# Kernel tuning notes

Hardware: AMD Instinct MI355X
Metric: run time of the kernel (lower is better)

Reference implementation:

```python
import jax, jax.numpy as jnp
import numpy as np

TOPK = 60            # candidates kept by top-k
THRESHOLD = 0.15     # score threshold (post-sigmoid)
NMS_THRESHOLD = 0.05 # IoU overlap for suppression/matching
NMS_TOPK = 20        # max kept detections per image
CROP_SIZE = (96, 96, 96)
AVG_TOPN = 7         # max matched boxes averaged per kept box


def setup_inputs() -> dict:
    key = jax.random.key(0)
    k1, k2, k3 = jax.random.split(key, 3)
    B, D, H, W = 256, 24, 24, 24
    Cls = jax.random.normal(k1, (B, 1, D, H, W), dtype=jnp.float32)
    # sizes in [1,7) voxels so 3D boxes at stride-4 anchor spacing overlap
    Shape = jax.random.uniform(k2, (B, 3, D, H, W), dtype=jnp.float32) * 6.0 + 1.0
    Offset = jax.random.normal(k3, (B, 3, D, H, W), dtype=jnp.float32)
    return {"Cls": Cls, "Shape": Shape, "Offset": Offset}


def _decode(Cls, Shape, Offset):
    # make_anchors + bbox_decode: centers = (anchor + offset) * stride, sizes = Shape
    B, _, D, H, W = Cls.shape
    stride = jnp.float32(CROP_SIZE[0] / D)  # 96/24 = 4
    gz, gy, gx = jnp.meshgrid(jnp.arange(D, dtype=jnp.float32),
                              jnp.arange(H, dtype=jnp.float32),
                              jnp.arange(W, dtype=jnp.float32), indexing="ij")
    anchors = jnp.stack([gz, gy, gx], -1).reshape(-1, 3)            # [N,3]
    scores = jax.nn.sigmoid(Cls.reshape(B, -1))                     # [B,N] (is_logits=True)
    shapes = Shape.reshape(B, 3, -1).transpose(0, 2, 1)             # [B,N,3]
    offsets = Offset.reshape(B, 3, -1).transpose(0, 2, 1)           # [B,N,3]
    centers = (anchors[None] + offsets) * stride
    bboxes = jnp.concatenate([centers, shapes], -1)                 # [B,N,6] = (z,y,x,d,h,w)
    return scores, bboxes


def _iou_matrix(det):
    # axis-aligned 3D IoU between all pairs of the TOPK candidate boxes
    c, s = det[:, 2:5], det[:, 5:8]
    lo, hi = c - 0.5 * s, c + 0.5 * s
    inter = jnp.prod(jnp.maximum(jnp.minimum(hi[:, None], hi[None]) -
                                 jnp.maximum(lo[:, None], lo[None]), 0.0), -1)
    vol = jnp.prod(s, -1)
    return inter / (vol[:, None] + vol[None] - inter)


def _nms_image(scores, bboxes):
    # top-k (sorted descending, as torch.topk) then masked iterative NMS with
    # IoU-matched top-7 box averaging, emitting a fixed [NMS_TOPK, 8] table.
    topk_s, topk_i = jax.lax.top_k(scores, TOPK)
    valid = topk_s > THRESHOLD
    det = jnp.concatenate([jnp.ones((TOPK, 1), jnp.float32),
                           topk_s[:, None], bboxes[topk_i]], -1)    # [TOPK,8]
    iou = _iou_matrix(det)
    ar = jnp.arange(TOPK)

    def step(suppressed, _):
        avail = valid & ~suppressed
        any_avail = jnp.any(avail)
        idx = jnp.argmax(avail)  # first available = highest remaining score
        matched = avail & ((iou[idx] > NMS_THRESHOLD) | (ar == idx))
        rank = jnp.cumsum(matched) - 1            # matched are already score-sorted
        sel = matched & (rank < AVG_TOPN)
        top_n = jnp.minimum(jnp.sum(matched), AVG_TOPN)
        avg = jnp.sum(det * sel[:, None].astype(det.dtype), 0) / jnp.maximum(top_n, 1).astype(det.dtype)
        avg = avg.at[0].set(1.0).at[1].set(det[idx, 1])  # flag=1, prob = best score
        row = jnp.where(top_n > 1, avg, det[idx])
        row = jnp.where(any_avail, row, -jnp.ones(8, det.dtype))
        suppressed = jnp.where(any_avail, suppressed | matched, suppressed)
        return suppressed, row

    _, rows = jax.lax.scan(step, jnp.zeros(TOPK, dtype=bool), None, length=NMS_TOPK)
    return rows  # [NMS_TOPK, 8]


def reference(Cls, Shape, Offset):
    scores, bboxes = _decode(Cls, Shape, Offset)
    return jax.vmap(_nms_image)(scores, bboxes)  # [B, NMS_TOPK, 8]
```

## Files before the change

### kernel.cpp

```cpp
#include <hip/hip_runtime.h>
#include <math.h>

#define N_ANCH 13824
#define TPB 256
#define K_TOP 60
#define K_NMS 20
#define AVG_TOPN 7
#define SLOTS 12
#define PIVOT_KEY 0xC0100000u

__device__ __forceinline__ unsigned mono_key(float x) {
  unsigned m = __float_as_uint(x);
  return (m & 0x80000000u) ? ~m : (m | 0x80000000u);
}

__global__ __launch_bounds__(TPB)
void detpp_kernel(const float* __restrict__ Cls,
                  const float* __restrict__ Shp,
                  const float* __restrict__ Off,
                  float* __restrict__ Out) {
  __shared__ unsigned long long cand2[TPB * SLOTS];
  __shared__ float det[K_TOP][9];
  __shared__ unsigned long long Mrow[K_TOP];
  __shared__ unsigned int hist[4][256];
  __shared__ unsigned long long cand[64];
  __shared__ unsigned long long selk[64];
  __shared__ unsigned int ccnt, totcnt, oflow;
  __shared__ unsigned int g_prefix, g_r;

  const int b = blockIdx.x;
  const int t = threadIdx.x;
  const int lane = t & 63;
  const size_t cbase = (size_t)b * N_ANCH;

  if (t == 0) { ccnt = 0; totcnt = 0; oflow = 0; g_prefix = 0u; g_r = K_TOP; }
  if (t < K_TOP) Mrow[t] = 1ull << t;
  hist[0][t] = 0; hist[1][t] = 0; hist[2][t] = 0; hist[3][t] = 0;

  const float4* C4 = (const float4*)(Cls + cbase);
  float4 v[14];
  #pragma unroll
  for (int j = 0; j < 13; ++j) v[j] = C4[(j << 8) + t];
  if (t < 128) v[13] = C4[3328 + t];

  int cnt = 0;
  const int base = t * SLOTS;
  auto process = [&](float4 val, int i0) {
    float a[4] = {val.x, val.y, val.z, val.w};
    #pragma unroll
    for (int q = 0; q < 4; ++q) {
      unsigned k = mono_key(a[q]);
      if (k > PIVOT_KEY) {
        if (cnt < SLOTS)
          cand2[base + cnt] = ((unsigned long long)k << 32) | (unsigned)(~(i0 + q));
        cnt++;
      }
    }
  };
  #pragma unroll
  for (int j = 0; j < 13; ++j) process(v[j], ((j << 8) + t) << 2);
  if (t < 128) process(v[13], (3328 + t) << 2);

  int wsum = cnt;
  #pragma unroll
  for (int d = 1; d < 64; d <<= 1) wsum += __shfl_xor(wsum, d, 64);
  unsigned long long ofm = __ballot(cnt > SLOTS);
  if (lane == 0) {
    atomicAdd(&totcnt, (unsigned)wsum);
    if (ofm) atomicOr(&oflow, 1u);
  }
  __syncthreads();
  const unsigned total = totcnt;
  const bool fast = (total >= (unsigned)K_TOP) && (oflow == 0u);
  const int myn = cnt < SLOTS ? cnt : SLOTS;

  #pragma unroll
  for (int pass = 0; pass < 4; ++pass) {
    const int shift = 24 - 8 * pass;
    const unsigned pref = g_prefix;
    const unsigned rr = g_r;
    if (fast) {
      for (int kk = 0; kk < myn; ++kk) {
        unsigned k = (unsigned)(cand2[base + kk] >> 32);
        bool match;
        if (pass == 0) match = true;
        else match = (((k ^ pref) >> (shift + 8)) == 0u);
        if (match) atomicAdd(&hist[pass][(k >> shift) & 0xffu], 1u);
      }
    } else {
      for (int j = 0; j < 54; ++j) {
        int i = (j << 8) | t;
        unsigned k = mono_key(Cls[cbase + i]);
        bool match;
        if (pass == 0) match = true;
        else match = (((k ^ pref) >> (shift + 8)) == 0u);
        if (match) atomicAdd(&hist[pass][(k >> shift) & 0xffu], 1u);
      }
    }
    __syncthreads();
    if (t < 64) {
      unsigned c0 = hist[pass][4 * lane + 0], c1 = hist[pass][4 * lane + 1];
      unsigned c2 = hist[pass][4 * lane + 2], c3 = hist[pass][4 * lane + 3];
      unsigned pre1 = c0, pre2 = c0 + c1, pre3 = pre2 + c2, pre4 = pre3 + c3;
      unsigned S = pre4;
      #pragma unroll
      for (int d = 1; d < 64; d <<= 1) {
        unsigned o = __shfl_down(S, d, 64);
        if (lane + d < 64) S += o;
      }
      unsigned pre[5] = {0u, pre1, pre2, pre3, pre4};
      int mybin = -1;
      #pragma unroll
      for (int kk = 3; kk >= 0; --kk) {
        if (mybin < 0 && S - pre[kk] >= rr) mybin = kk;
      }
      unsigned long long m = __ballot(mybin >= 0);
      int hl = 63 - __builtin_clzll(m);
      if (lane == hl) {
        g_prefix = pref | ((unsigned)(4 * lane + mybin) << shift);
        g_r = rr - (S - pre[mybin + 1]);
      }
    }
    __syncthreads();
  }

  const unsigned K60 = g_prefix;
  if (fast) {
    for (int kk = 0; kk < myn; ++kk) {
      unsigned long long e = cand2[base + kk];
      if ((unsigned)(e >> 32) >= K60) {
        unsigned pos = atomicAdd(&ccnt, 1u);
        if (pos < 64) cand[pos] = e;
      }
    }
  } else {
    for (int j = 0; j < 54; ++j) {
      int i = (j << 8) | t;
      unsigned k = mono_key(Cls[cbase + i]);
      if (k >= K60) {
        unsigned pos = atomicAdd(&ccnt, 1u);
        if (pos < 64) cand[pos] = ((unsigned long long)k << 32) | (unsigned)(~i);
      }
    }
  }
  __syncthreads();

  if (t < 64) {
    unsigned cc = ccnt; if (cc > 64u) cc = 64u;
    unsigned long long klong = (lane < (int)cc) ? cand[lane] : 0ull;
    unsigned long long vv = ~klong;
    #pragma unroll
    for (int k = 2; k <= 64; k <<= 1) {
      #pragma unroll
      for (int j = k >> 1; j > 0; j >>= 1) {
        unsigned long long o = __shfl_xor(vv, j, 64);
        bool i_lower = ((lane & j) == 0);
        bool asc = ((lane & k) == 0);
        bool keep_min = (asc == i_lower);
        bool take = keep_min ? (o < vv) : (o > vv);
        if (take) vv = o;
      }
    }
    selk[lane] = ~vv;
  }
  __syncthreads();

  if (t < 180) {
    int e = t / 3;
    int f = t - 3 * e;
    unsigned long long kl = selk[e];
    int i = (int)(~(unsigned)(kl & 0xffffffffull));
    int iz = i / 576;
    int r2 = i - iz * 576;
    int iy = r2 / 24;
    int ix = r2 - iy * 24;
    int a = (f == 0) ? iz : ((f == 1) ? iy : ix);
    size_t bb = (size_t)b * 3 * N_ANCH + (size_t)f * N_ANCH + (size_t)i;
    float o = Off[bb];
    float s = Shp[bb];
    det[e][2 + f] = ((float)a + o) * 4.0f;
    det[e][5 + f] = s;
  } else if (t < 240) {
    int e = t - 180;
    unsigned long long kl = selk[e];
    unsigned m = (unsigned)(kl >> 32);
    unsigned bits = (m & 0x80000000u) ? (m & 0x7fffffffu) : ~m;
    float lg = __uint_as_float(bits);
    det[e][0] = 1.0f;
    det[e][1] = 1.0f / (1.0f + expf(-lg));
  }
  __syncthreads();

  for (int p = t; p < 1800; p += TPB) {
    int ii = p / 30;
    int k  = p - ii * 30;
    int jj = ii + 1 + k; if (jj >= 60) jj -= 60;
    float cz1 = det[ii][2], cy1 = det[ii][3], cx1 = det[ii][4];
    float sz1 = det[ii][5], sy1 = det[ii][6], sx1 = det[ii][7];
    float cz2 = det[jj][2], cy2 = det[jj][3], cx2 = det[jj][4];
    float sz2 = det[jj][5], sy2 = det[jj][6], sx2 = det[jj][7];
    float lz1 = cz1 - 0.5f * sz1, hz1 = cz1 + 0.5f * sz1;
    float ly1 = cy1 - 0.5f * sy1, hy1 = cy1 + 0.5f * sy1;
    float lx1 = cx1 - 0.5f * sx1, hx1 = cx1 + 0.5f * sx1;
    float lz2 = cz2 - 0.5f * sz2, hz2 = cz2 + 0.5f * sz2;
    float ly2 = cy2 - 0.5f * sy2, hy2 = cy2 + 0.5f * sy2;
    float lx2 = cx2 - 0.5f * sx2, hx2 = cx2 + 0.5f * sx2;
    float dz = fmaxf(fminf(hz1, hz2) - fmaxf(lz1, lz2), 0.0f);
    float dy = fmaxf(fminf(hy1, hy2) - fmaxf(ly1, ly2), 0.0f);
    float dx = fmaxf(fminf(hx1, hx2) - fmaxf(lx1, lx2), 0.0f);
    float inter = (dz * dy) * dx;
    float v1 = (sz1 * sy1) * sx1;
    float v2 = (sz2 * sy2) * sx2;
    float iouv = inter / (v1 + v2 - inter);
    if (iouv > 0.05f) {
      atomicOr(&Mrow[ii], 1ull << jj);
      atomicOr(&Mrow[jj], 1ull << ii);
    }
  }
  __syncthreads();

  if (t < 64) {
    const bool in = (lane < K_TOP);
    float myscore = in ? det[lane][1] : 0.0f;
    unsigned long long M = in ? Mrow[lane] : 0ull;
    unsigned long long validm = __ballot(in && (myscore > 0.15f));
    unsigned long long suppressed = 0ull;
    float* outb = Out + (size_t)b * K_NMS * 8;
    const int q = lane >> 3, c = lane & 7;

    #pragma unroll
    for (int step = 0; step < K_NMS; ++step) {
      unsigned long long avail = validm & ~suppressed;
      const bool any = (avail != 0ull);
      int idx = any ? (int)__builtin_ctzll(avail) : 0;
      unsigned mlo = (unsigned)__builtin_amdgcn_readlane((int)(unsigned)(M & 0xffffffffull), idx);
      unsigned mhi = (unsigned)__builtin_amdgcn_readlane((int)(unsigned)(M >> 32), idx);
      unsigned long long matched = any ? (avail & (((unsigned long long)mhi << 32) | mlo)) : 0ull;
      int cm = __popcll(matched);
      int top_n = cm < AVG_TOPN ? cm : AVG_TOPN;
      int myb = 0;
      { unsigned long long m2 = matched;
        #pragma unroll
        for (int z = 0; z < 8; ++z) {
          int bz = m2 ? (int)__builtin_ctzll(m2) : 0;
          if (z == q) myb = bz;
          m2 &= m2 - 1ull;
        } }
      float vv = (q < top_n) ? det[myb][c] : 0.0f;
      vv += __shfl_xor(vv, 8, 64);
      vv += __shfl_xor(vv, 16, 64);
      vv += __shfl_xor(vv, 32, 64);
      float sidx = __uint_as_float((unsigned)__builtin_amdgcn_readlane((int)__float_as_uint(myscore), idx));
      float r = vv / (float)(top_n > 0 ? top_n : 1);
      if (lane < 8) {
        float o = r;
        if (lane == 0) o = 1.0f;
        if (lane == 1) o = sidx;
        if (!any) o = -1.0f;
        outb[step * 8 + lane] = o;
      }
      suppressed |= matched;
    }
  }
}

extern "C" void kernel_launch(void* const* d_in, const int* in_sizes, int n_in,
                              void* d_out, int out_size, void* d_ws, size_t ws_size,
                              hipStream_t stream) {
  const float* Cls = (const float*)d_in[0];
  const float* Shp = (const float*)d_in[1];
  const float* Off = (const float*)d_in[2];
  float* Out = (float*)d_out;
  int B = in_sizes[0] / N_ANCH;
  detpp_kernel<<<B, TPB, 0, stream>>>(Cls, Shp, Off, Out);
}
```

Baseline: 123.2 us.

## Replace radix-select top-k with compacted candidate list and rank-by-count selection

Raises the block to 1024 threads and compacts every above-pivot logit into one shared list using a wave prefix scan, with a single atomic per wave. The four-pass histogram radix select and bitonic sort are replaced by rank counting: each candidate counts how many list entries beat it and writes its decoded box straight to that rank if it ranks below 60. This removes several barrier-separated passes and shared-memory histogram atomics. In exchange the counting is quadratic in the list size, and the fallback path is an O(N²) global-memory scan that would be very slow if ever taken.

```diff
diff --git a/kernel.cpp b/kernel.cpp
--- a/kernel.cpp
+++ b/kernel.cpp
@@ -2,11 +2,11 @@
 #include <math.h>
 
 #define N_ANCH 13824
-#define TPB 256
+#define TPB 1024
 #define K_TOP 60
 #define K_NMS 20
 #define AVG_TOPN 7
-#define SLOTS 12
+#define CAP 2048
 #define PIVOT_KEY 0xC0100000u
 
 __device__ __forceinline__ unsigned mono_key(float x) {
@@ -19,182 +19,129 @@
                   const float* __restrict__ Shp,
                   const float* __restrict__ Off,
                   float* __restrict__ Out) {
-  __shared__ unsigned long long cand2[TPB * SLOTS];
+  __shared__ unsigned long long list[CAP];
   __shared__ float det[K_TOP][9];
   __shared__ unsigned long long Mrow[K_TOP];
-  __shared__ unsigned int hist[4][256];
-  __shared__ unsigned long long cand[64];
-  __shared__ unsigned long long selk[64];
-  __shared__ unsigned int ccnt, totcnt, oflow;
-  __shared__ unsigned int g_prefix, g_r;
+  __shared__ unsigned int cnt2;
 
   const int b = blockIdx.x;
   const int t = threadIdx.x;
   const int lane = t & 63;
   const size_t cbase = (size_t)b * N_ANCH;
 
-  if (t == 0) { ccnt = 0; totcnt = 0; oflow = 0; g_prefix = 0u; g_r = K_TOP; }
+  if (t == 0) cnt2 = 0;
   if (t < K_TOP) Mrow[t] = 1ull << t;
-  hist[0][t] = 0; hist[1][t] = 0; hist[2][t] = 0; hist[3][t] = 0;
 
   const float4* C4 = (const float4*)(Cls + cbase);
-  float4 v[14];
+  float4 v0 = C4[t];
+  float4 v1 = C4[1024 + t];
+  float4 v2 = C4[2048 + t];
+  const bool tail = (t < 384);
+  float4 v3 = tail ? C4[3072 + t] : make_float4(0.f, 0.f, 0.f, 0.f);
+  __syncthreads();
+
+  unsigned k[16];
+  k[0]  = mono_key(v0.x); k[1]  = mono_key(v0.y); k[2]  = mono_key(v0.z); k[3]  = mono_key(v0.w);
+  k[4]  = mono_key(v1.x); k[5]  = mono_key(v1.y); k[6]  = mono_key(v1.z); k[7]  = mono_key(v1.w);
+  k[8]  = mono_key(v2.x); k[9]  = mono_key(v2.y); k[10] = mono_key(v2.z); k[11] = mono_key(v2.w);
+  if (tail) {
+    k[12] = mono_key(v3.x); k[13] = mono_key(v3.y); k[14] = mono_key(v3.z); k[15] = mono_key(v3.w);
+  } else {
+    k[12] = 0u; k[13] = 0u; k[14] = 0u; k[15] = 0u;
+  }
+
+  int cnt = 0;
   #pragma unroll
-  for (int j = 0; j < 13; ++j) v[j] = C4[(j << 8) + t];
-  if (t < 128) v[13] = C4[3328 + t];
-
-  int cnt = 0;
-  const int base = t * SLOTS;
-  auto process = [&](float4 val, int i0) {
-    float a[4] = {val.x, val.y, val.z, val.w};
+  for (int q = 0; q < 16; ++q) cnt += (k[q] > PIVOT_KEY) ? 1 : 0;
+
+  int pfx = cnt;
+  #pragma unroll
+  for (int d = 1; d < 64; d <<= 1) {
+    int o = __shfl_up(pfx, d, 64);
+    if (lane >= d) pfx += o;
+  }
+  const int excl = pfx - cnt;
+  int wtot = __shfl(pfx, 63, 64);
+  unsigned wbase = 0;
+  if (lane == 63) wbase = atomicAdd(&cnt2, (unsigned)wtot);
+  wbase = (unsigned)__shfl((int)wbase, 63, 64);
+
+  {
+    int off = (int)wbase + excl;
     #pragma unroll
-    for (int q = 0; q < 4; ++q) {
-      unsigned k = mono_key(a[q]);
-      if (k > PIVOT_KEY) {
-        if (cnt < SLOTS)
-          cand2[base + cnt] = ((unsigned long long)k << 32) | (unsigned)(~(i0 + q));
-        cnt++;
-      }
-    }
-  };
-  #pragma unroll
-  for (int j = 0; j < 13; ++j) process(v[j], ((j << 8) + t) << 2);
-  if (t < 128) process(v[13], (3328 + t) << 2);
-
-  int wsum = cnt;
-  #pragma unroll
-  for (int d = 1; d < 64; d <<= 1) wsum += __shfl_xor(wsum, d, 64);
-  unsigned long long ofm = __ballot(cnt > SLOTS);
-  if (lane == 0) {
-    atomicAdd(&totcnt, (unsigned)wsum);
-    if (ofm) atomicOr(&oflow, 1u);
-  }
-  __syncthreads();
-  const unsigned total = totcnt;
-  const bool fast = (total >= (unsigned)K_TOP) && (oflow == 0u);
-  const int myn = cnt < SLOTS ? cnt : SLOTS;
-
-  #pragma unroll
-  for (int pass = 0; pass < 4; ++pass) {
-    const int shift = 24 - 8 * pass;
-    const unsigned pref = g_prefix;
-    const unsigned rr = g_r;
-    if (fast) {
-      for (int kk = 0; kk < myn; ++kk) {
-        unsigned k = (unsigned)(cand2[base + kk] >> 32);
-        bool match;
-        if (pass == 0) match = true;
-        else match = (((k ^ pref) >> (shift + 8)) == 0u);
-        if (match) atomicAdd(&hist[pass][(k >> shift) & 0xffu], 1u);
-      }
-    } else {
-      for (int j = 0; j < 54; ++j) {
-        int i = (j << 8) | t;
-        unsigned k = mono_key(Cls[cbase + i]);
-        bool match;
-        if (pass == 0) match = true;
-        else match = (((k ^ pref) >> (shift + 8)) == 0u);
-        if (match) atomicAdd(&hist[pass][(k >> shift) & 0xffu], 1u);
-      }
-    }
-    __syncthreads();
-    if (t < 64) {
-      unsigned c0 = hist[pass][4 * lane + 0], c1 = hist[pass][4 * lane + 1];
-      unsigned c2 = hist[pass][4 * lane + 2], c3 = hist[pass][4 * lane + 3];
-      unsigned pre1 = c0, pre2 = c0 + c1, pre3 = pre2 + c2, pre4 = pre3 + c3;
-      unsigned S = pre4;
-      #pragma unroll
-      for (int d = 1; d < 64; d <<= 1) {
-        unsigned o = __shfl_down(S, d, 64);
-        if (lane + d < 64) S += o;
-      }
-      unsigned pre[5] = {0u, pre1, pre2, pre3, pre4};
-      int mybin = -1;
-      #pragma unroll
-      for (int kk = 3; kk >= 0; --kk) {
-        if (mybin < 0 && S - pre[kk] >= rr) mybin = kk;
-      }
-      unsigned long long m = __ballot(mybin >= 0);
-      int hl = 63 - __builtin_clzll(m);
-      if (lane == hl) {
-        g_prefix = pref | ((unsigned)(4 * lane + mybin) << shift);
-        g_r = rr - (S - pre[mybin + 1]);
-      }
-    }
-    __syncthreads();
-  }
-
-  const unsigned K60 = g_prefix;
-  if (fast) {
-    for (int kk = 0; kk < myn; ++kk) {
-      unsigned long long e = cand2[base + kk];
-      if ((unsigned)(e >> 32) >= K60) {
-        unsigned pos = atomicAdd(&ccnt, 1u);
-        if (pos < 64) cand[pos] = e;
-      }
-    }
-  } else {
-    for (int j = 0; j < 54; ++j) {
-      int i = (j << 8) | t;
-      unsigned k = mono_key(Cls[cbase + i]);
-      if (k >= K60) {
-        unsigned pos = atomicAdd(&ccnt, 1u);
-        if (pos < 64) cand[pos] = ((unsigned long long)k << 32) | (unsigned)(~i);
-      }
-    }
-  }
-  __syncthreads();
-
-  if (t < 64) {
-    unsigned cc = ccnt; if (cc > 64u) cc = 64u;
-    unsigned long long klong = (lane < (int)cc) ? cand[lane] : 0ull;
-    unsigned long long vv = ~klong;
-    #pragma unroll
-    for (int k = 2; k <= 64; k <<= 1) {
-      #pragma unroll
-      for (int j = k >> 1; j > 0; j >>= 1) {
-        unsigned long long o = __shfl_xor(vv, j, 64);
-        bool i_lower = ((lane & j) == 0);
-        bool asc = ((lane & k) == 0);
-        bool keep_min = (asc == i_lower);
-        bool take = keep_min ? (o < vv) : (o > vv);
-        if (take) vv = o;
-      }
-    }
-    selk[lane] = ~vv;
-  }
-  __syncthreads();
-
-  if (t < 180) {
-    int e = t / 3;
-    int f = t - 3 * e;
-    unsigned long long kl = selk[e];
-    int i = (int)(~(unsigned)(kl & 0xffffffffull));
+    for (int q = 0; q < 16; ++q) {
+      if (k[q] > PIVOT_KEY) {
+        int base_i = (q < 4) ? (t << 2) : (q < 8) ? ((1024 + t) << 2)
+                     : (q < 12) ? ((2048 + t) << 2) : ((3072 + t) << 2);
+        int i = base_i + (q & 3);
+        if (off < CAP)
+          list[off] = ((unsigned long long)k[q] << 32) | (unsigned)(~i);
+        off++;
+      }
+    }
+  }
+  __syncthreads();
+
+  const unsigned total = cnt2;
+  const bool fast = (total >= (unsigned)K_TOP) && (total <= (unsigned)CAP);
+
+  auto build_det = [&](unsigned long long e, int r) {
+    int i = (int)(~(unsigned)(e & 0xffffffffull));
+    unsigned m = (unsigned)(e >> 32);
+    unsigned bits = (m & 0x80000000u) ? (m & 0x7fffffffu) : ~m;
+    float lg = __uint_as_float(bits);
+    float sc = 1.0f / (1.0f + expf(-lg));
     int iz = i / 576;
     int r2 = i - iz * 576;
     int iy = r2 / 24;
     int ix = r2 - iy * 24;
-    int a = (f == 0) ? iz : ((f == 1) ? iy : ix);
-    size_t bb = (size_t)b * 3 * N_ANCH + (size_t)f * N_ANCH + (size_t)i;
-    float o = Off[bb];
-    float s = Shp[bb];
-    det[e][2 + f] = ((float)a + o) * 4.0f;
-    det[e][5 + f] = s;
-  } else if (t < 240) {
-    int e = t - 180;
-    unsigned long long kl = selk[e];
-    unsigned m = (unsigned)(kl >> 32);
-    unsigned bits = (m & 0x80000000u) ? (m & 0x7fffffffu) : ~m;
-    float lg = __uint_as_float(bits);
-    det[e][0] = 1.0f;
-    det[e][1] = 1.0f / (1.0f + expf(-lg));
+    size_t bb = (size_t)b * 3 * N_ANCH + (size_t)i;
+    float o0 = Off[bb], o1 = Off[bb + N_ANCH], o2 = Off[bb + 2 * N_ANCH];
+    float s0 = Shp[bb], s1 = Shp[bb + N_ANCH], s2 = Shp[bb + 2 * N_ANCH];
+    det[r][0] = 1.0f;
+    det[r][1] = sc;
+    det[r][2] = ((float)iz + o0) * 4.0f;
+    det[r][3] = ((float)iy + o1) * 4.0f;
+    det[r][4] = ((float)ix + o2) * 4.0f;
+    det[r][5] = s0;
+    det[r][6] = s1;
+    det[r][7] = s2;
+  };
+
+  if (fast) {
+    if (t < (int)total) {
+      const unsigned long long e = list[t];
+      int r = 0;
+      int j = 0;
+      const int tot = (int)total;
+      for (; j + 4 <= tot; j += 4) {
+        r += (list[j]     > e) ? 1 : 0;
+        r += (list[j + 1] > e) ? 1 : 0;
+        r += (list[j + 2] > e) ? 1 : 0;
+        r += (list[j + 3] > e) ? 1 : 0;
+      }
+      for (; j < tot; ++j) r += (list[j] > e) ? 1 : 0;
+      if (r < K_TOP) build_det(e, r);
+    }
+  } else {
+    for (int i = t; i < N_ANCH; i += TPB) {
+      unsigned ki = mono_key(Cls[cbase + i]);
+      unsigned long long e = ((unsigned long long)ki << 32) | (unsigned)(~i);
+      int r = 0;
+      for (int j = 0; j < N_ANCH; ++j) {
+        unsigned kj = mono_key(Cls[cbase + j]);
+        unsigned long long ej = ((unsigned long long)kj << 32) | (unsigned)(~j);
+        r += (ej > e) ? 1 : 0;
+      }
+      if (r < K_TOP) build_det(e, r);
+    }
   }
   __syncthreads();
 
   for (int p = t; p < 1800; p += TPB) {
     int ii = p / 30;
-    int k  = p - ii * 30;
-    int jj = ii + 1 + k; if (jj >= 60) jj -= 60;
+    int kk = p - ii * 30;
+    int jj = ii + 1 + kk; if (jj >= 60) jj -= 60;
     float cz1 = det[ii][2], cy1 = det[ii][3], cx1 = det[ii][4];
     float sz1 = det[ii][5], sy1 = det[ii][6], sx1 = det[ii][7];
     float cz2 = det[jj][2], cy2 = det[jj][3], cx2 = det[jj][4];
```

Result: faster. 117.8 us (-4.4%).
